# Kernel tuning notes

Measured on AMD Instinct MI355X. Metric: run time of the kernel, lower is better.

## Reference

```python
import jax, jax.numpy as jnp
import numpy as np

B, T, D_IN = 4, 4096, 1024
H, DK, DV, D_MODEL = 16, 64, 64, 1024
EPS = 1e-6


def setup_inputs() -> dict:
    key = jax.random.key(0)
    ks = jax.random.split(key, 11)
    s_in = 1.0 / np.sqrt(D_IN)
    s_o = 1.0 / np.sqrt(H * DV)
    return {
        "query": jax.random.normal(ks[0], (B, T, D_IN), jnp.float32),
        "key": jax.random.normal(ks[1], (B, T, D_IN), jnp.float32),
        "value": jax.random.normal(ks[2], (B, T, D_IN), jnp.float32),
        "Wq": jax.random.normal(ks[3], (D_IN, H * DK), jnp.float32) * s_in,
        "bq": jnp.zeros((H * DK,), jnp.float32),
        "Wk": jax.random.normal(ks[4], (D_IN, H * DK), jnp.float32) * s_in,
        "bk": jnp.zeros((H * DK,), jnp.float32),
        "Wv": jax.random.normal(ks[5], (D_IN, H * DV), jnp.float32) * s_in,
        "bv": jnp.zeros((H * DV,), jnp.float32),
        "Wo": jax.random.normal(ks[6], (H * DV, D_MODEL), jnp.float32) * s_o,
        "bo": jnp.zeros((D_MODEL,), jnp.float32),
    }


def _phi(x):
    # ELU(x) + 1 feature map (positive kernel feature)
    return jax.nn.elu(x) + 1.0


def reference(query, key, value, Wq, bq, Wk, bk, Wv, bv, Wo, bo):
    b, t, _ = query.shape
    q = _phi(query @ Wq + bq).reshape(b, t, H, DK)   # [B,T,H,DK]
    k = _phi(key @ Wk + bk).reshape(b, t, H, DK)     # [B,T,H,DK]
    v = (value @ Wv + bv).reshape(b, t, H, DV)       # [B,T,H,DV]
    # KV accumulation over time: [B,H,DV,DK]
    kv = jnp.einsum('bthd,bthk->bhkd', k, v)
    # normalizer: q . sum_t(k)  -> [B,T,H]
    norm = 1.0 / (jnp.einsum('bthd,bhd->bth', q, k.sum(axis=1)) + EPS)
    attn = jnp.einsum('bthd,bhkd,bth->bthk', q, kv, norm)  # [B,T,H,DV]
    attn = attn.reshape(b, t, H * DV)
    return attn @ Wo + bo
```

## Files before the change

kernel.cpp:

```cpp
#include <hip/hip_runtime.h>

typedef __bf16 bf16;
typedef bf16 bf16x2 __attribute__((ext_vector_type(2)));
typedef bf16 bf16x8 __attribute__((ext_vector_type(8)));
typedef float f32x4 __attribute__((ext_vector_type(4)));

#define B_ 4
#define T_ 4096
#define H_ 16
#define DK_ 64
#define DV_ 64
#define DMODEL_ 1024
#define M_ (B_ * T_)
#define EPS_ 1e-6f

#define BARX()  asm volatile("s_barrier" ::: "memory")
#define LGKM0() asm volatile("s_waitcnt lgkmcnt(0)" ::: "memory")

__device__ __forceinline__ void async_ld16(const void* g, void* l) {
    __builtin_amdgcn_global_load_lds(
        (const __attribute__((address_space(1))) unsigned int*)g,
        (__attribute__((address_space(3))) unsigned int*)l,
        16, 0, 0);
}

struct TPtrs { const float* s[4]; bf16* d[4]; };

__global__ void transpose4(TPtrs p) {
    __shared__ bf16 t[32][33];
    const float* src = p.s[blockIdx.z];
    bf16*        dst = p.d[blockIdx.z];
    const int tx = threadIdx.x, ty = threadIdx.y;
    const int x  = blockIdx.x * 32 + tx;
    const int y0 = blockIdx.y * 32 + ty;
#pragma unroll
    for (int i = 0; i < 32; i += 8)
        t[ty + i][tx] = (bf16)src[(size_t)(y0 + i) * 1024 + x];
    __syncthreads();
    const int xo = blockIdx.y * 32 + tx;
    const int yo = blockIdx.x * 32 + ty;
#pragma unroll
    for (int i = 0; i < 32; i += 8)
        dst[(size_t)(yo + i) * 1024 + xo] = t[tx][ty + i];
}

__global__ __launch_bounds__(256) void cvt_kernel(
    const float* __restrict__ src, bf16* __restrict__ dst)
{
    const size_t i = (size_t)blockIdx.x * 256 + threadIdx.x;
    const float4* s = (const float4*)src + 2 * i;
    float4 a = s[0];
    float4 b = s[1];
    bf16x8 h;
    h[0] = (bf16)a.x; h[1] = (bf16)a.y; h[2] = (bf16)a.z; h[3] = (bf16)a.w;
    h[4] = (bf16)b.x; h[5] = (bf16)b.y; h[6] = (bf16)b.z; h[7] = (bf16)b.w;
    *(bf16x8*)(dst + 8 * i) = h;
}


__device__ __forceinline__ void stage_half(
    const bf16* __restrict__ G, int base_rc, int K,
    char* lds_op_buf, int t, int h, int w, int lane)
{
    const int r8   = lane >> 3;
    const int row  = h * 128 + w * 8 + r8;
    const int cole = (((lane & 7) ^ r8) << 3);
    const bf16* g = G + (size_t)(base_rc + row) * K + t * 64 + cole;
    char* l = lds_op_buf + h * 16384 + w * 1024;
    async_ld16(g, l);
    async_ld16(g + (size_t)64 * K, l + 8192);
}

template<int G>
__device__ __forceinline__ void read_a4(bf16x8 (&aF)[4][2], const char* ab,
                                        int arow, int fq, int l7) {
#pragma unroll
    for (int i = 0; i < 4; ++i)
#pragma unroll
        for (int ks = 0; ks < 2; ++ks)
            aF[i][ks] = *(const bf16x8*)(ab
                + (arow + (G * 4 + i) * 16) * 128
                + ((((ks << 2) + fq) ^ l7) << 4));
}

template<int JP>
__device__ __forceinline__ void read_b2(bf16x8 (&bF)[4][2], const char* bb,
                                        int brow, int fq, int l7) {
#pragma unroll
    for (int j = 0; j < 2; ++j)
#pragma unroll
        for (int ks = 0; ks < 2; ++ks)
            bF[JP * 2 + j][ks] = *(const bf16x8*)(bb
                + (brow + (JP * 2 + j) * 16) * 128
                + ((((ks << 2) + fq) ^ l7) << 4));
}

template<int G, int JP>
__device__ __forceinline__ void mfma_q(f32x4 (&acc)[8][4],
                                       const bf16x8 (&aF)[4][2],
                                       const bf16x8 (&bF)[4][2]) {
#pragma unroll
    for (int i = 0; i < 4; ++i)
#pragma unroll
        for (int j = 0; j < 2; ++j)
#pragma unroll
            for (int ks = 0; ks < 2; ++ks)
                acc[G * 4 + i][JP * 2 + j] =
                    __builtin_amdgcn_mfma_f32_16x16x32_bf16(
                        aF[i][ks], bF[JP * 2 + j][ks],
                        acc[G * 4 + i][JP * 2 + j], 0, 0, 0);
}

template<int ACT, int F32OUT>
__global__ __launch_bounds__(512, 2) void gemm256_kernel(
    const bf16* __restrict__ A, const bf16* __restrict__ Bt,
    const float* __restrict__ bias, void* __restrict__ Cout,
    int M, int N, int K)
{
    __shared__ f32x4 smem4[8192];
    char* smem = (char*)smem4;
    char* Ab0 = smem;
    char* Ab1 = smem + 32768;
    char* Bb0 = smem + 65536;
    char* Bb1 = smem + 98304;

    const int tid  = threadIdx.x;
    const int w    = tid >> 6, lane = tid & 63;
    const int wrow = w >> 2,  wcol = w & 3;
    const int fr = lane & 15, fq = lane >> 4, l7 = lane & 7;
    const int arow = wrow * 128 + fr;
    const int brow = wcol * 64 + fr;

    const int nwg  = gridDim.x * gridDim.y;
    const int flat = blockIdx.y * gridDim.x + blockIdx.x;
    const int swz  = (flat & 7) * (nwg >> 3) + (flat >> 3);
    const int n0   = (swz % gridDim.x) * 256;
    const int m0   = (swz / gridDim.x) * 256;

    const int KT = K >> 6;

    f32x4  acc[8][4] = {};
    bf16x8 aF[4][2], bF[4][2];

    stage_half(Bt, n0, K, Bb0, 0, 0, w, lane);
    stage_half(Bt, n0, K, Bb0, 0, 1, w, lane);
    stage_half(A,  m0, K, Ab0, 0, 0, w, lane);
    stage_half(A,  m0, K, Ab0, 0, 1, w, lane);
    stage_half(Bt, n0, K, Bb1, 1, 0, w, lane);
    stage_half(Bt, n0, K, Bb1, 1, 1, w, lane);
    stage_half(A,  m0, K, Ab1, 1, 0, w, lane);
    stage_half(A,  m0, K, Ab1, 1, 1, w, lane);
    asm volatile("s_waitcnt vmcnt(8)" ::: "memory");
    BARX();

    for (int it = 0; it < (KT >> 1); ++it) {
        const int  t0   = it * 2, t1 = t0 + 1;
        const bool more = (it < (KT >> 1) - 1);

        read_a4<0>(aF, Ab0, arow, fq, l7);
        read_b2<0>(bF, Bb0, brow, fq, l7);
        asm volatile("s_waitcnt lgkmcnt(8)" ::: "memory");
        BARX(); LGKM0();
        __builtin_amdgcn_s_setprio(1);
        mfma_q<0, 0>(acc, aF, bF);
        __builtin_amdgcn_s_setprio(0);
        BARX();

        read_b2<1>(bF, Bb0, brow, fq, l7);
        BARX(); LGKM0();
        __builtin_amdgcn_s_setprio(1);
        mfma_q<0, 1>(acc, aF, bF);
        __builtin_amdgcn_s_setprio(0);
        BARX();

        read_a4<1>(aF, Ab0, arow, fq, l7);
        if (more) {
            stage_half(Bt, n0, K, Bb0, t0 + 2, 0, w, lane);
            stage_half(Bt, n0, K, Bb0, t0 + 2, 1, w, lane);
        }
        BARX(); LGKM0();
        __builtin_amdgcn_s_setprio(1);
        mfma_q<1, 0>(acc, aF, bF);
        __builtin_amdgcn_s_setprio(0);
        BARX();

        if (more) {
            stage_half(A, m0, K, Ab0, t0 + 2, 0, w, lane);
            stage_half(A, m0, K, Ab0, t0 + 2, 1, w, lane);
            asm volatile("s_waitcnt vmcnt(8)" ::: "memory");
        } else {
            asm volatile("s_waitcnt vmcnt(0)" ::: "memory");
        }
        BARX();
        __builtin_amdgcn_s_setprio(1);
        mfma_q<1, 1>(acc, aF, bF);
        __builtin_amdgcn_s_setprio(0);
        BARX();

        read_a4<0>(aF, Ab1, arow, fq, l7);
        read_b2<0>(bF, Bb1, brow, fq, l7);
        asm volatile("s_waitcnt lgkmcnt(8)" ::: "memory");
        BARX(); LGKM0();
        __builtin_amdgcn_s_setprio(1);
        mfma_q<0, 0>(acc, aF, bF);
        __builtin_amdgcn_s_setprio(0);
        BARX();

        read_b2<1>(bF, Bb1, brow, fq, l7);
        BARX(); LGKM0();
        __builtin_amdgcn_s_setprio(1);
        mfma_q<0, 1>(acc, aF, bF);
        __builtin_amdgcn_s_setprio(0);
        BARX();

        read_a4<1>(aF, Ab1, arow, fq, l7);
        if (more) {
            stage_half(Bt, n0, K, Bb1, t1 + 2, 0, w, lane);
            stage_half(Bt, n0, K, Bb1, t1 + 2, 1, w, lane);
        }
        BARX(); LGKM0();
        __builtin_amdgcn_s_setprio(1);
        mfma_q<1, 0>(acc, aF, bF);
        __builtin_amdgcn_s_setprio(0);
        BARX();

        if (more) {
            stage_half(A, m0, K, Ab1, t1 + 2, 0, w, lane);
            stage_half(A, m0, K, Ab1, t1 + 2, 1, w, lane);
            asm volatile("s_waitcnt vmcnt(8)" ::: "memory");
        }
        BARX();
        __builtin_amdgcn_s_setprio(1);
        mfma_q<1, 1>(acc, aF, bF);
        __builtin_amdgcn_s_setprio(0);
        BARX();
    }

    const size_t Ns = (size_t)N;
#pragma unroll
    for (int g = 0; g < 8; ++g) {
#pragma unroll
        for (int j = 0; j < 4; ++j) {
            const int col = n0 + wcol * 64 + j * 16 + fr;
            const float bb = bias[col];
            const int row0 = m0 + wrow * 128 + g * 16 + fq * 4;
#pragma unroll
            for (int r = 0; r < 4; ++r) {
                float x = acc[g][j][r] + bb;
                if (ACT) x = (x > 0.0f) ? (x + 1.0f) : __expf(x);
                if (F32OUT)
                    ((float*)Cout)[(size_t)(row0 + r) * Ns + col] = x;
                else
                    ((bf16*)Cout)[(size_t)(row0 + r) * Ns + col] = (bf16)x;
            }
        }
    }
}

__global__ __launch_bounds__(256) void kv_partial_kernel(
    const bf16* __restrict__ Kb, const bf16* __restrict__ V,
    float* __restrict__ kv_part, float* __restrict__ ksum_part)
{
    const int bh = blockIdx.y;
    const int b  = bh >> 4;
    const int h  = bh & 15;
    const int tc = blockIdx.x;
    const int TC = T_ / 8;
    const int t0 = tc * TC;

    __shared__ float kb[8][64];
    __shared__ float vb[8][64];

    const int tid = threadIdx.x;
    const int dvq = tid >> 4;
    const int dkq = tid & 15;
    const int lr  = tid >> 5;
    const int lc  = (tid & 31) << 1;

    float acc[4][4] = {};
    float ksacc = 0.0f;

    for (int tt0 = 0; tt0 < TC; tt0 += 8) {
        const size_t base = ((size_t)(b * T_) + t0 + tt0 + lr) * 1024 + h * 64 + lc;
        bf16x2 k2 = *(const bf16x2*)&Kb[base];
        bf16x2 v2 = *(const bf16x2*)&V[base];
        kb[lr][lc] = (float)k2[0]; kb[lr][lc + 1] = (float)k2[1];
        vb[lr][lc] = (float)v2[0]; vb[lr][lc + 1] = (float)v2[1];
        __syncthreads();
#pragma unroll
        for (int tt = 0; tt < 8; ++tt) {
            float4 vv = *(const float4*)&vb[tt][dvq * 4];
            float4 kk = *(const float4*)&kb[tt][dkq * 4];
            float va[4] = {vv.x, vv.y, vv.z, vv.w};
            float ka[4] = {kk.x, kk.y, kk.z, kk.w};
#pragma unroll
            for (int i = 0; i < 4; ++i)
#pragma unroll
                for (int j = 0; j < 4; ++j)
                    acc[i][j] += va[i] * ka[j];
        }
        if (tid < 64) {
#pragma unroll
            for (int tt = 0; tt < 8; ++tt) ksacc += kb[tt][tid];
        }
        __syncthreads();
    }

    float* kvp = kv_part + ((size_t)tc * 64 + bh) * 4096;
#pragma unroll
    for (int i = 0; i < 4; ++i) {
        float4 wv = make_float4(acc[i][0], acc[i][1], acc[i][2], acc[i][3]);
        *(float4*)&kvp[(dvq * 4 + i) * 64 + dkq * 4] = wv;
    }
    if (tid < 64)
        ksum_part[((size_t)tc * 64 + bh) * 64 + tid] = ksacc;
}

__global__ __launch_bounds__(256) void kv_reduce_kernel(
    const float* __restrict__ kv_part, const float* __restrict__ ksum_part,
    bf16* __restrict__ kvb, float* __restrict__ ksum)
{
    const int bh = blockIdx.x;
    const int tid = threadIdx.x;
    for (int e = tid; e < 4096; e += 256) {
        float s = 0.0f;
#pragma unroll
        for (int tc = 0; tc < 8; ++tc)
            s += kv_part[((size_t)tc * 64 + bh) * 4096 + e];
        kvb[(size_t)bh * 4096 + e] = (bf16)s;
    }
    if (tid < 64) {
        float s = 0.0f;
#pragma unroll
        for (int tc = 0; tc < 8; ++tc)
            s += ksum_part[((size_t)tc * 64 + bh) * 64 + tid];
        ksum[bh * 64 + tid] = s;
    }
}

__global__ __launch_bounds__(256) void attn_kernel(
    const bf16* __restrict__ Q, const bf16* __restrict__ kvb,
    const float* __restrict__ ksum, bf16* __restrict__ attn)
{
    const int bh = blockIdx.y;
    const int b  = bh >> 4;
    const int h  = bh & 15;
    const int t0 = blockIdx.x * 128;

    __shared__ bf16 As[128 * 64];
    __shared__ bf16 Bs[64 * 64];
    __shared__ float ksum_s[64];
    __shared__ float norm_s[128];

    const int tid  = threadIdx.x;
    const int wave = tid >> 6;
    const int lane = tid & 63;

    const bf16* Qbase = Q + ((size_t)(b * T_) + t0) * 1024 + h * 64;

#pragma unroll
    for (int r2 = 0; r2 < 4; ++r2) {
        const int c   = r2 * 256 + wave * 64 + lane;
        const int row = c >> 3;
        const int ko  = (c & 7) * 8;
        char* l = (char*)As + (size_t)(r2 * 256 + wave * 64) * 16;
        async_ld16(Qbase + (size_t)row * 1024 + ko, l);
    }
    {
        const float4* src = (const float4*)(kvb + (size_t)bh * 4096);
        float4* dst = (float4*)Bs;
        for (int e = tid; e < 512; e += 256) dst[e] = src[e];
    }
    if (tid < 64) ksum_s[tid] = ksum[bh * 64 + tid];
    __syncthreads();

    if (tid < 128) {
        float s = 0.0f;
#pragma unroll
        for (int u = 0; u < 8; ++u) {
            const int slot = (u + tid) & 7;
            bf16x8 v = *(const bf16x8*)&As[tid * 64 + slot * 8];
#pragma unroll
            for (int e = 0; e < 8; ++e) s += (float)v[e] * ksum_s[slot * 8 + e];
        }
        norm_s[tid] = 1.0f / (s + EPS_);
    }
    __syncthreads();

    const int fr  = lane & 15;
    const int fkq = lane >> 4;
    f32x4 acc[2][4] = {};
#pragma unroll
    for (int ks = 0; ks < 2; ++ks) {
        bf16x8 af[2], bfr[4];
#pragma unroll
        for (int i = 0; i < 2; ++i)
            af[i] = *(const bf16x8*)&As[(wave * 32 + i * 16 + fr) * 64 + ks * 32 + fkq * 8];
#pragma unroll
        for (int j = 0; j < 4; ++j)
            bfr[j] = *(const bf16x8*)&Bs[(j * 16 + fr) * 64 + ks * 32 + fkq * 8];
#pragma unroll
        for (int i = 0; i < 2; ++i)
#pragma unroll
            for (int j = 0; j < 4; ++j)
                acc[i][j] = __builtin_amdgcn_mfma_f32_16x16x32_bf16(
                    af[i], bfr[j], acc[i][j], 0, 0, 0);
    }

    bf16* out = attn + ((size_t)(b * T_) + t0) * 1024 + h * 64;
#pragma unroll
    for (int i = 0; i < 2; ++i)
#pragma unroll
        for (int j = 0; j < 4; ++j)
#pragma unroll
            for (int r = 0; r < 4; ++r) {
                const int row = wave * 32 + i * 16 + fkq * 4 + r;
                const int col = j * 16 + fr;
                out[(size_t)row * 1024 + col] = (bf16)(acc[i][j][r] * norm_s[row]);
            }
}

extern "C" void kernel_launch(void* const* d_in, const int* in_sizes, int n_in,
                              void* d_out, int out_size, void* d_ws, size_t ws_size,
                              hipStream_t stream) {
    const float* query = (const float*)d_in[0];
    const float* key_  = (const float*)d_in[1];
    const float* value = (const float*)d_in[2];
    const float* Wq = (const float*)d_in[3];
    const float* bq = (const float*)d_in[4];
    const float* Wk = (const float*)d_in[5];
    const float* bk = (const float*)d_in[6];
    const float* Wv = (const float*)d_in[7];
    const float* bv = (const float*)d_in[8];
    const float* Wo = (const float*)d_in[9];
    const float* bo = (const float*)d_in[10];

    char* ws = (char*)d_ws;
    char* out8 = (char*)d_out;
    const size_t MB = 1024 * 1024;
    bf16* WqT = (bf16*)(ws + 0 * MB);
    bf16* WkT = (bf16*)(ws + 2 * MB);
    bf16* WvT = (bf16*)(ws + 4 * MB);
    bf16* WoT = (bf16*)(ws + 6 * MB);
    bf16* CVT = (bf16*)(ws + 8 * MB);
    float* kv_part   = (float*)(ws + 40 * MB);
    float* ksum_part = (float*)(ws + 48 * MB);
    bf16*  kvb  = (bf16*)(ws + 48 * MB + 128 * 1024);
    float* ksum = (float*)(ws + 48 * MB + 640 * 1024);

    bf16* KB   = (bf16*)out8;
    bf16* VB   = (bf16*)(out8 + 32 * MB);
    bf16* Qb   = (bf16*)out8;
    bf16* ATTN = CVT;

    TPtrs tp;
    tp.s[0] = Wq;  tp.s[1] = Wk;  tp.s[2] = Wv;  tp.s[3] = Wo;
    tp.d[0] = WqT; tp.d[1] = WkT; tp.d[2] = WvT; tp.d[3] = WoT;
    transpose4<<<dim3(32, 32, 4), dim3(32, 8, 1), 0, stream>>>(tp);

    const int CVT_BLOCKS = M_ * 1024 / 8 / 256;
    const dim3 G256(4, 64);

    cvt_kernel<<<CVT_BLOCKS, 256, 0, stream>>>(key_, CVT);
    gemm256_kernel<1, 0><<<G256, 512, 0, stream>>>(CVT, WkT, bk, KB, M_, 1024, 1024);

    cvt_kernel<<<CVT_BLOCKS, 256, 0, stream>>>(value, CVT);
    gemm256_kernel<0, 0><<<G256, 512, 0, stream>>>(CVT, WvT, bv, VB, M_, 1024, 1024);

    kv_partial_kernel<<<dim3(8, 64), 256, 0, stream>>>(KB, VB, kv_part, ksum_part);
    kv_reduce_kernel<<<dim3(64), 256, 0, stream>>>(kv_part, ksum_part, kvb, ksum);

    cvt_kernel<<<CVT_BLOCKS, 256, 0, stream>>>(query, CVT);
    gemm256_kernel<1, 0><<<G256, 512, 0, stream>>>(CVT, WqT, bq, Qb, M_, 1024, 1024);

    attn_kernel<<<dim3(32, 64), 256, 0, stream>>>(Qb, kvb, ksum, ATTN);

    gemm256_kernel<0, 1><<<G256, 512, 0, stream>>>(ATTN, WoT, bo, (float*)d_out, M_, 1024, 1024);
}
```

Baseline: 448.9 us.

## Emit K/V transposed from GEMM and compute KV partials with MFMA

The K and V projection GEMMs now write their outputs transposed (feature-major, time-contiguous) through a swizzled LDS staging epilogue. With that layout the kv_partial kernel stages tiles with async global-to-LDS loads and double buffering, then accumulates K^T V using bf16 MFMA instead of scalar FP32 FMAs. The aim is to cut the cost of the KV accumulation stage, which was a scalar outer-product loop. In exchange, the GEMM epilogue gains an extra LDS round trip and barrier, and its global stores become strided column writes.

```diff
diff --git a/kernel.cpp b/kernel.cpp
--- a/kernel.cpp
+++ b/kernel.cpp
@@ -111,7 +111,7 @@
                         acc[G * 4 + i][JP * 2 + j], 0, 0, 0);
 }
 
-template<int ACT, int F32OUT>
+template<int ACT, int OUTMODE>
 __global__ __launch_bounds__(512, 2) void gemm256_kernel(
     const bf16* __restrict__ A, const bf16* __restrict__ Bt,
     const float* __restrict__ bias, void* __restrict__ Cout,
@@ -237,83 +237,138 @@
     }
 
     const size_t Ns = (size_t)N;
-#pragma unroll
-    for (int g = 0; g < 8; ++g) {
-#pragma unroll
-        for (int j = 0; j < 4; ++j) {
-            const int col = n0 + wcol * 64 + j * 16 + fr;
-            const float bb = bias[col];
-            const int row0 = m0 + wrow * 128 + g * 16 + fq * 4;
-#pragma unroll
-            for (int r = 0; r < 4; ++r) {
-                float x = acc[g][j][r] + bb;
-                if (ACT) x = (x > 0.0f) ? (x + 1.0f) : __expf(x);
-                if (F32OUT)
-                    ((float*)Cout)[(size_t)(row0 + r) * Ns + col] = x;
-                else
-                    ((bf16*)Cout)[(size_t)(row0 + r) * Ns + col] = (bf16)x;
+    if constexpr (OUTMODE == 2) {
+        __syncthreads();
+        char* eb = smem;
+#pragma unroll
+        for (int g = 0; g < 8; ++g)
+#pragma unroll
+            for (int j = 0; j < 4; ++j) {
+                const int col = wcol * 64 + j * 16 + fr;
+                const float bb = bias[n0 + col];
+#pragma unroll
+                for (int r = 0; r < 4; ++r) {
+                    float x = acc[g][j][r] + bb;
+                    if (ACT) x = (x > 0.0f) ? (x + 1.0f) : __expf(x);
+                    const int row = wrow * 128 + g * 16 + fq * 4 + r;
+                    *(bf16*)(eb + row * 512
+                        + ((((col >> 3) ^ (row & 7)) << 4) | ((col & 7) << 1)))
+                        = (bf16)x;
+                }
             }
+        __syncthreads();
+        bf16* Cp = (bf16*)Cout;
+#pragma unroll
+        for (int o = 0; o < 16; ++o) {
+            const int n = (tid >> 3) + (o & 3) * 64;
+            const int m = (tid & 7) * 8 + (o >> 2) * 64;
+            bf16x8 v;
+#pragma unroll
+            for (int e = 0; e < 8; ++e) {
+                const int row = m + e;
+                v[e] = *(const bf16*)(eb + row * 512
+                        + ((((n >> 3) ^ (row & 7)) << 4) | ((n & 7) << 1)));
+            }
+            *(bf16x8*)(Cp + (size_t)(n0 + n) * M + m0 + m) = v;
+        }
+    } else {
+#pragma unroll
+        for (int g = 0; g < 8; ++g) {
+#pragma unroll
+            for (int j = 0; j < 4; ++j) {
+                const int col = n0 + wcol * 64 + j * 16 + fr;
+                const float bb = bias[col];
+                const int row0 = m0 + wrow * 128 + g * 16 + fq * 4;
+#pragma unroll
+                for (int r = 0; r < 4; ++r) {
+                    float x = acc[g][j][r] + bb;
+                    if (ACT) x = (x > 0.0f) ? (x + 1.0f) : __expf(x);
+                    if (OUTMODE == 1)
+                        ((float*)Cout)[(size_t)(row0 + r) * Ns + col] = x;
+                    else
+                        ((bf16*)Cout)[(size_t)(row0 + r) * Ns + col] = (bf16)x;
+                }
+            }
         }
     }
 }
 
 __global__ __launch_bounds__(256) void kv_partial_kernel(
-    const bf16* __restrict__ Kb, const bf16* __restrict__ V,
+    const bf16* __restrict__ KT, const bf16* __restrict__ VT,
     float* __restrict__ kv_part, float* __restrict__ ksum_part)
 {
-    const int bh = blockIdx.y;
-    const int b  = bh >> 4;
-    const int h  = bh & 15;
+    const int bh = blockIdx.y, b = bh >> 4, h = bh & 15;
     const int tc = blockIdx.x;
-    const int TC = T_ / 8;
-    const int t0 = tc * TC;
-
-    __shared__ float kb[8][64];
-    __shared__ float vb[8][64];
-
-    const int tid = threadIdx.x;
-    const int dvq = tid >> 4;
-    const int dkq = tid & 15;
-    const int lr  = tid >> 5;
-    const int lc  = (tid & 31) << 1;
-
-    float acc[4][4] = {};
-    float ksacc = 0.0f;
-
-    for (int tt0 = 0; tt0 < TC; tt0 += 8) {
-        const size_t base = ((size_t)(b * T_) + t0 + tt0 + lr) * 1024 + h * 64 + lc;
-        bf16x2 k2 = *(const bf16x2*)&Kb[base];
-        bf16x2 v2 = *(const bf16x2*)&V[base];
-        kb[lr][lc] = (float)k2[0]; kb[lr][lc + 1] = (float)k2[1];
-        vb[lr][lc] = (float)v2[0]; vb[lr][lc + 1] = (float)v2[1];
-        __syncthreads();
-#pragma unroll
-        for (int tt = 0; tt < 8; ++tt) {
-            float4 vv = *(const float4*)&vb[tt][dvq * 4];
-            float4 kk = *(const float4*)&kb[tt][dkq * 4];
-            float va[4] = {vv.x, vv.y, vv.z, vv.w};
-            float ka[4] = {kk.x, kk.y, kk.z, kk.w};
-#pragma unroll
-            for (int i = 0; i < 4; ++i)
-#pragma unroll
-                for (int j = 0; j < 4; ++j)
-                    acc[i][j] += va[i] * ka[j];
-        }
-        if (tid < 64) {
-#pragma unroll
-            for (int tt = 0; tt < 8; ++tt) ksacc += kb[tt][tid];
-        }
-        __syncthreads();
+    __shared__ char lds[32768];
+
+    const int tid = threadIdx.x, wv = tid >> 6, lane = tid & 63;
+    const int fr = lane & 15, fq = lane >> 4, l7 = lane & 7;
+
+    const int r1 = wv * 8 + (lane >> 3);
+    const int c1 = ((lane & 7) ^ (r1 & 7)) << 3;
+    const size_t g1 = (size_t)(h * 64 + r1) * M_ + (size_t)b * T_ + c1;
+    const size_t g2 = g1 + (size_t)32 * M_;
+    const int dstoff = (wv * 64 + lane) * 16;
+
+    f32x4 acc[4] = {};
+    float ksa = 0.0f;
+    const int rk = tid >> 2, qk = tid & 3;
+
+    {
+        const size_t mo = (size_t)tc * 512;
+        async_ld16(VT + g1 + mo, lds + dstoff);
+        async_ld16(VT + g2 + mo, lds + 4096 + dstoff);
+        async_ld16(KT + g1 + mo, lds + 8192 + dstoff);
+        async_ld16(KT + g2 + mo, lds + 12288 + dstoff);
+    }
+    for (int it = 0; it < 8; ++it) {
+        char* cur = lds + (it & 1) * 16384;
+        char* nxt = lds + ((it & 1) ^ 1) * 16384;
+        if (it < 7) {
+            const size_t mo = (size_t)tc * 512 + (it + 1) * 64;
+            async_ld16(VT + g1 + mo, nxt + dstoff);
+            async_ld16(VT + g2 + mo, nxt + 4096 + dstoff);
+            async_ld16(KT + g1 + mo, nxt + 8192 + dstoff);
+            async_ld16(KT + g2 + mo, nxt + 12288 + dstoff);
+            asm volatile("s_waitcnt vmcnt(4)" ::: "memory");
+        } else {
+            asm volatile("s_waitcnt vmcnt(0)" ::: "memory");
+        }
+        BARX();
+        const char* Vb = cur;
+        const char* Kb = cur + 8192;
+#pragma unroll
+        for (int ks = 0; ks < 2; ++ks) {
+            bf16x8 av = *(const bf16x8*)(Vb + (wv * 16 + fr) * 128
+                        + ((((ks << 2) + fq) ^ l7) << 4));
+#pragma unroll
+            for (int j = 0; j < 4; ++j) {
+                bf16x8 bk = *(const bf16x8*)(Kb + (j * 16 + fr) * 128
+                            + ((((ks << 2) + fq) ^ l7) << 4));
+                acc[j] = __builtin_amdgcn_mfma_f32_16x16x32_bf16(
+                    av, bk, acc[j], 0, 0, 0);
+            }
+        }
+        {
+            bf16x8 s0 = *(const bf16x8*)(Kb + rk * 128 + (((2 * qk) ^ (rk & 7)) << 4));
+            bf16x8 s1 = *(const bf16x8*)(Kb + rk * 128 + (((2 * qk + 1) ^ (rk & 7)) << 4));
+#pragma unroll
+            for (int e = 0; e < 8; ++e) ksa += (float)s0[e] + (float)s1[e];
+        }
+        BARX();
     }
 
     float* kvp = kv_part + ((size_t)tc * 64 + bh) * 4096;
 #pragma unroll
-    for (int i = 0; i < 4; ++i) {
-        float4 wv = make_float4(acc[i][0], acc[i][1], acc[i][2], acc[i][3]);
-        *(float4*)&kvp[(dvq * 4 + i) * 64 + dkq * 4] = wv;
-    }
-    if (tid < 64)
-        ksum_part[((size_t)tc * 64 + bh) * 64 + tid] = ksacc;
+    for (int j = 0; j < 4; ++j)
+#pragma unroll
+        for (int r = 0; r < 4; ++r)
+            kvp[(wv * 16 + fq * 4 + r) * 64 + j * 16 + fr] = acc[j][r];
+
+    float s = ksa;
+    s += __shfl_xor(s, 1);
+    s += __shfl_xor(s, 2);
+    if (qk == 0) ksum_part[((size_t)tc * 64 + bh) * 64 + rk] = s;
 }
 
 __global__ __launch_bounds__(256) void kv_reduce_kernel(
@@ -448,8 +503,8 @@
     bf16*  kvb  = (bf16*)(ws + 48 * MB + 128 * 1024);
     float* ksum = (float*)(ws + 48 * MB + 640 * 1024);
 
-    bf16* KB   = (bf16*)out8;
-    bf16* VB   = (bf16*)(out8 + 32 * MB);
+    bf16* KTg  = (bf16*)out8;
+    bf16* VTg  = (bf16*)(out8 + 32 * MB);
     bf16* Qb   = (bf16*)out8;
     bf16* ATTN = CVT;
 
@@ -462,12 +517,12 @@
     const dim3 G256(4, 64);
 
     cvt_kernel<<<CVT_BLOCKS, 256, 0, stream>>>(key_, CVT);
-    gemm256_kernel<1, 0><<<G256, 512, 0, stream>>>(CVT, WkT, bk, KB, M_, 1024, 1024);
+    gemm256_kernel<1, 2><<<G256, 512, 0, stream>>>(CVT, WkT, bk, KTg, M_, 1024, 1024);
 
     cvt_kernel<<<CVT_BLOCKS, 256, 0, stream>>>(value, CVT);
-    gemm256_kernel<0, 0><<<G256, 512, 0, stream>>>(CVT, WvT, bv, VB, M_, 1024, 1024);
-
-    kv_partial_kernel<<<dim3(8, 64), 256, 0, stream>>>(KB, VB, kv_part, ksum_part);
+    gemm256_kernel<0, 2><<<G256, 512, 0, stream>>>(CVT, WvT, bv, VTg, M_, 1024, 1024);
+
+    kv_partial_kernel<<<dim3(8, 64), 256, 0, stream>>>(KTg, VTg, kv_part, ksum_part);
     kv_reduce_kernel<<<dim3(64), 256, 0, stream>>>(kv_part, ksum_part, kvb, ksum);
 
     cvt_kernel<<<CVT_BLOCKS, 256, 0, stream>>>(query, CVT);
```

After: 425.2 us. -5.3%, faster.
